# Kernel optimization log

Measured on AMD Instinct MI355X. Metric: run time of the kernel, lower is better.

Reference implementation:

```python
import jax, jax.numpy as jnp
import numpy as np

D_MODEL = 1024
N_HEADS = 16
N_KV_HEADS = 4
D_K = D_MODEL // N_HEADS  # 64
GROUPS = N_HEADS // N_KV_HEADS
GATE_IN = 12
Q_SIZE = D_MODEL
KV_SIZE = N_KV_HEADS * D_K
QKV_SIZE = Q_SIZE + 2 * KV_SIZE
ROPE_BASE = 10000.0


def rms_norm(x, w):
    # torch nn.RMSNorm with eps=None -> finfo(dtype).eps
    eps = jnp.finfo(x.dtype).eps
    var = jnp.mean(x * x, axis=-1, keepdims=True)
    return x * jax.lax.rsqrt(var + eps) * w


def rope(x):
    # torchtune RotaryPositionalEmbeddings: interleaved pairs. x: [B,S,H,D]
    B, S, H, D = x.shape
    half = D // 2
    theta = 1.0 / (ROPE_BASE ** (jnp.arange(0, half, dtype=jnp.float32) * 2.0 / D))
    ang = jnp.arange(S, dtype=jnp.float32)[:, None] * theta[None, :]  # [S, half]
    cos = jnp.cos(ang)[None, :, None, :]
    sin = jnp.sin(ang)[None, :, None, :]
    xp = x.reshape(B, S, H, half, 2)
    x0, x1 = xp[..., 0], xp[..., 1]
    out = jnp.stack([x0 * cos - x1 * sin, x1 * cos + x0 * sin], axis=-1)
    return out.reshape(B, S, H, D).astype(x.dtype)


def setup_inputs() -> dict:
    key = jax.random.key(0)
    k1, k2, k3, k4, k5 = jax.random.split(key, 5)
    B, S = 2, 2048
    x = jax.random.normal(k1, (B, S, D_MODEL), dtype=jnp.float32)
    qkvo_proj = 0.02 * jax.random.normal(k2, (QKV_SIZE + D_MODEL, D_MODEL), dtype=jnp.float32)
    q_norm_w = jnp.ones((D_K,), dtype=jnp.float32) + 0.01 * jax.random.normal(k3, (D_K,), dtype=jnp.float32)
    k_norm_w = jnp.ones((D_K,), dtype=jnp.float32) + 0.01 * jax.random.normal(k4, (D_K,), dtype=jnp.float32)
    gate_w = 0.02 * jax.random.normal(k5, (N_HEADS, GATE_IN), dtype=jnp.float32)
    return {"x": x, "qkvo_proj": qkvo_proj, "q_norm_w": q_norm_w,
            "k_norm_w": k_norm_w, "gate_w": gate_w}


def reference(x, qkvo_proj, q_norm_w, k_norm_w, gate_w):
    B, S, _ = x.shape
    qkv = jnp.einsum('bsd,ed->bse', x, qkvo_proj[:QKV_SIZE])
    Q = qkv[..., :Q_SIZE].reshape(B, S, N_HEADS, D_K)
    K = qkv[..., Q_SIZE:Q_SIZE + KV_SIZE].reshape(B, S, N_KV_HEADS, D_K)
    V = qkv[..., Q_SIZE + KV_SIZE:].reshape(B, S, N_KV_HEADS, D_K)
    Q = rope(rms_norm(Q, q_norm_w))
    K = rope(rms_norm(K, k_norm_w))
    # GQA: repeat kv heads (repeat_interleave along head dim)
    K = jnp.repeat(K, GROUPS, axis=2)
    V = jnp.repeat(V, GROUPS, axis=2)
    scale = 1.0 / jnp.sqrt(jnp.float32(D_K))
    scores = jnp.einsum('bqhd,bkhd->bhqk', Q, K) * scale
    causal = jnp.tril(jnp.ones((S, S), dtype=bool))
    scores = jnp.where(causal[None, None], scores, jnp.float32(-jnp.inf))
    probs = jax.nn.softmax(scores, axis=-1)
    attn = jnp.einsum('bhqk,bkhd->bqhd', probs, V)  # [B,S,H,D_K]
    gate = jax.nn.sigmoid(jnp.einsum('bsg,hg->bsh', x[..., :GATE_IN], gate_w))
    attn = attn * gate[..., None]
    attn = attn.reshape(B, S, D_MODEL)
    return jnp.einsum('bsd,ed->bse', attn, qkvo_proj[QKV_SIZE:])
```

## Files before the change

### kernel.cpp

```cpp
#include <hip/hip_runtime.h>
#include <math.h>

typedef unsigned short u16;
typedef unsigned int u32;
typedef __bf16 bf16x8 __attribute__((ext_vector_type(8)));
typedef float f32x4 __attribute__((ext_vector_type(4)));
typedef unsigned short u16x8 __attribute__((ext_vector_type(8)));
typedef unsigned int u32x2 __attribute__((ext_vector_type(2)));

static __device__ __forceinline__ u16 f2bf(float f) {
  unsigned int u = __builtin_bit_cast(unsigned int, f);
  u = (u + 0x7FFFu + ((u >> 16) & 1u)) >> 16;
  return (u16)u;
}
static __device__ __forceinline__ float bf2f(u16 u) {
  unsigned int x = ((unsigned int)u) << 16;
  return __builtin_bit_cast(float, x);
}
static __device__ __forceinline__ u16 f2bfh(float f) {
  __bf16 b = (__bf16)f;
  return __builtin_bit_cast(u16, b);
}
static __device__ __forceinline__ void gll16(const u16* g, u16* l) {
  __builtin_amdgcn_global_load_lds((const __attribute__((address_space(1))) u32*)g,
                                   (__attribute__((address_space(3))) u32*)l, 16, 0, 0);
}

#define QSCALE 0.18033688011112042f

__global__ __launch_bounds__(256) void prep_k(const float* __restrict__ a, u16* __restrict__ da, int n4a,
                                              const float* __restrict__ b, u16* __restrict__ db, int n4b,
                                              float2* __restrict__ tab) {
  int idx = blockIdx.x * 256 + threadIdx.x;
  if (idx < n4a + n4b) {
    const float* src; u16* dst; int i;
    if (idx < n4a) { src = a; dst = da; i = idx; }
    else { src = b; dst = db; i = idx - n4a; }
    float4 v = ((const float4*)src)[i];
    ushort4 r;
    r.x = f2bf(v.x); r.y = f2bf(v.y); r.z = f2bf(v.z); r.w = f2bf(v.w);
    ((ushort4*)dst)[i] = r;
  } else {
    int e = idx - n4a - n4b;
    if (e < 2048 * 32) {
      int s = e >> 5, j = e & 31;
      float sn, cs;
      sincosf((float)s * expf(-(float)j * (9.21034037198f / 32.0f)), &sn, &cs);
      tab[e] = make_float2(cs, sn);
    }
  }
}

__global__ __launch_bounds__(256) void gemm_nt(const u16* __restrict__ A, const u16* __restrict__ B,
                                               float* __restrict__ C, int M, int N, int K) {
  __shared__ __align__(16) u16 sA[64 * 32];
  __shared__ __align__(16) u16 sB[128 * 32];
  const int tid = threadIdx.x;
  const int w = tid >> 6, lane = tid & 63, l15 = lane & 15;
  const int m0 = blockIdx.x * 64, n0 = blockIdx.y * 128;
  const int wm = (w >> 1) * 32, wn = (w & 1) * 64;

  f32x4 acc[2][4] = {};

  int sArow, sAcol;
  {
    int p = tid * 16;
    int row = p >> 6, oo = p & 63;
    int ol = oo ^ (((row >> 1) & 3) << 4);
    sArow = row; sAcol = ol >> 1;
  }
  int sBrow[2], sBcol[2];
#pragma unroll
  for (int i = 0; i < 2; ++i) {
    int p = i * 4096 + tid * 16;
    int row = p >> 6, oo = p & 63;
    int ol = oo ^ (((row >> 1) & 3) << 4);
    sBrow[i] = row; sBcol[i] = ol >> 1;
  }
  int aoff[2], boff[4];
  const int kb = (lane >> 4) * 16;
#pragma unroll
  for (int m = 0; m < 2; ++m) {
    int r = wm + m * 16 + l15;
    aoff[m] = r * 64 + (kb ^ (((r >> 1) & 3) << 4));
  }
#pragma unroll
  for (int n = 0; n < 4; ++n) {
    int r = wn + n * 16 + l15;
    boff[n] = r * 64 + (kb ^ (((r >> 1) & 3) << 4));
  }

  for (int k0 = 0; k0 < K; k0 += 32) {
    gll16(A + (size_t)(m0 + sArow) * K + k0 + sAcol, (u16*)((char*)sA + tid * 16));
#pragma unroll
    for (int i = 0; i < 2; ++i)
      gll16(B + (size_t)(n0 + sBrow[i]) * K + k0 + sBcol[i], (u16*)((char*)sB + i * 4096 + tid * 16));
    __syncthreads();
    bf16x8 af[2], bfr[4];
#pragma unroll
    for (int m = 0; m < 2; ++m) af[m] = *(const bf16x8*)((const char*)sA + aoff[m]);
#pragma unroll
    for (int n = 0; n < 4; ++n) bfr[n] = *(const bf16x8*)((const char*)sB + boff[n]);
#pragma unroll
    for (int m = 0; m < 2; ++m)
#pragma unroll
      for (int n = 0; n < 4; ++n)
        acc[m][n] = __builtin_amdgcn_mfma_f32_16x16x32_bf16(af[m], bfr[n], acc[m][n], 0, 0, 0);
    __syncthreads();
  }

#pragma unroll
  for (int m = 0; m < 2; ++m)
#pragma unroll
    for (int i = 0; i < 4; ++i) {
      int gr = m0 + wm + m * 16 + (lane >> 4) * 4 + i;
      float* crow = C + (size_t)gr * N + n0 + wn + l15;
#pragma unroll
      for (int n = 0; n < 4; ++n) crow[n * 16] = acc[m][n][i];
    }
}

__global__ __launch_bounds__(256) void gemm_qkv(const u16* __restrict__ A, const u16* __restrict__ B,
                                                const float* __restrict__ qw, const float* __restrict__ kw,
                                                const float2* __restrict__ tab,
                                                u16* __restrict__ Qo, u16* __restrict__ Ko,
                                                u16* __restrict__ Vt, int K) {
  __shared__ __align__(16) u16 sA[64 * 32];
  __shared__ __align__(16) u16 sB[128 * 32];
  const int tid = threadIdx.x;
  const int w = tid >> 6, lane = tid & 63, l15 = lane & 15, lg = lane >> 4;
  const int m0 = blockIdx.x * 64, n0 = blockIdx.y * 128;
  const int wm = (w >> 1) * 32, wn = (w & 1) * 64;

  f32x4 acc[2][4] = {};

  int sArow, sAcol;
  {
    int p = tid * 16;
    int row = p >> 6, oo = p & 63;
    int ol = oo ^ (((row >> 1) & 3) << 4);
    sArow = row; sAcol = ol >> 1;
  }
  int sBrow[2], sBcol[2];
#pragma unroll
  for (int i = 0; i < 2; ++i) {
    int p = i * 4096 + tid * 16;
    int row = p >> 6, oo = p & 63;
    int ol = oo ^ (((row >> 1) & 3) << 4);
    sBrow[i] = row; sBcol[i] = ol >> 1;
  }
  int aoff[2], boff[4];
  const int kb = lg * 16;
#pragma unroll
  for (int m = 0; m < 2; ++m) {
    int r = wm + m * 16 + l15;
    aoff[m] = r * 64 + (kb ^ (((r >> 1) & 3) << 4));
  }
#pragma unroll
  for (int n = 0; n < 4; ++n) {
    int r = wn + n * 16 + l15;
    boff[n] = r * 64 + (kb ^ (((r >> 1) & 3) << 4));
  }

  for (int k0 = 0; k0 < K; k0 += 32) {
    gll16(A + (size_t)(m0 + sArow) * K + k0 + sAcol, (u16*)((char*)sA + tid * 16));
#pragma unroll
    for (int i = 0; i < 2; ++i)
      gll16(B + (size_t)(n0 + sBrow[i]) * K + k0 + sBcol[i], (u16*)((char*)sB + i * 4096 + tid * 16));
    __syncthreads();
    bf16x8 af[2], bfr[4];
#pragma unroll
    for (int m = 0; m < 2; ++m) af[m] = *(const bf16x8*)((const char*)sA + aoff[m]);
#pragma unroll
    for (int n = 0; n < 4; ++n) bfr[n] = *(const bf16x8*)((const char*)sB + boff[n]);
#pragma unroll
    for (int m = 0; m < 2; ++m)
#pragma unroll
      for (int n = 0; n < 4; ++n)
        acc[m][n] = __builtin_amdgcn_mfma_f32_16x16x32_bf16(af[m], bfr[n], acc[m][n], 0, 0, 0);
    __syncthreads();
  }

  const int he = (n0 + wn) >> 6;
  if (he < 20) {
    const float* wnorm = (he < 16) ? qw : kw;
    const float oscale = (he < 16) ? QSCALE : 1.0f;
    float wv[4];
#pragma unroll
    for (int n = 0; n < 4; ++n) wv[n] = wnorm[n * 16 + l15];
    float2 tj[4];
#pragma unroll
    for (int m = 0; m < 2; ++m)
#pragma unroll
      for (int i = 0; i < 4; ++i) {
        const int gr = m0 + wm + m * 16 + lg * 4 + i;
        const int s = gr & 2047, bb = gr >> 11;
        float ss = 0.f;
#pragma unroll
        for (int n = 0; n < 4; ++n) ss += acc[m][n][i] * acc[m][n][i];
        ss += __shfl_xor(ss, 8); ss += __shfl_xor(ss, 4);
        ss += __shfl_xor(ss, 2); ss += __shfl_xor(ss, 1);
        const float r = rsqrtf(ss * (1.0f / 64.0f) + 1.1920929e-7f);
#pragma unroll
        for (int n = 0; n < 4; ++n) tj[n] = tab[s * 32 + n * 8 + (l15 >> 1)];
        u16* orow = (he < 16)
          ? Qo + ((size_t)(bb * 16 + he) * 2048 + s) * 64 + l15
          : Ko + ((size_t)(bb * 4 + (he - 16)) * 2048 + s) * 64 + l15;
#pragma unroll
        for (int n = 0; n < 4; ++n) {
          float xn = acc[m][n][i] * r * wv[n];
          float p = __shfl_xor(xn, 1);
          float outv = ((l15 & 1) == 0) ? (xn * tj[n].x - p * tj[n].y)
                                        : (xn * tj[n].x + p * tj[n].y);
          orow[n * 16] = f2bf(outv * oscale);
        }
      }
  } else {
#pragma unroll
    for (int m = 0; m < 2; ++m)
#pragma unroll
      for (int i = 0; i < 4; ++i) {
        const int gr = m0 + wm + m * 16 + lg * 4 + i;
        const int s = gr & 2047, bb = gr >> 11;
        u16* vcol = Vt + ((size_t)(bb * 4 + (he - 20)) * 64 + l15) * 2048 + s;
#pragma unroll
        for (int n = 0; n < 4; ++n) vcol[(size_t)n * 16 * 2048] = f2bf(acc[m][n][i]);
      }
  }
}

__global__ __launch_bounds__(256) void attn_fwd_pair(const u16* __restrict__ Q, const u16* __restrict__ Kg,
                                                     const u16* __restrict__ Vt,
                                                     u16* __restrict__ accP, float* __restrict__ lP) {
  __shared__ __align__(16) u16 sK[64 * 64];
  __shared__ __align__(16) u16 sV[64 * 64];
  __shared__ __align__(16) u16 sP[4][16 * 64];

  const int tid = threadIdx.x;
  const int w = tid >> 6, lane = tid & 63;
  const int l15 = lane & 15, lg = lane >> 4;
  const int qiA = blockIdx.x;
  const int qiB = 31 - qiA;
  const int z = blockIdx.z;
  const int bh = blockIdx.y, b = bh >> 4, h = bh & 15, kvh = h >> 2;

  const u16* Qp = Q + (size_t)(b * 16 + h) * 2048 * 64;
  const u16* Kp = Kg + (size_t)(b * 4 + kvh) * 2048 * 64;
  const u16* Vp = Vt + (size_t)(b * 4 + kvh) * 64 * 2048;

  const int q0s[2] = {qiA * 64, qiB * 64};
  bf16x8 qa[2][2];
#pragma unroll
  for (int s = 0; s < 2; ++s) {
    const u16* qrow = Qp + (size_t)(q0s[s] + w * 16 + l15) * 64 + lg * 8;
    qa[s][0] = *(const bf16x8*)qrow;
    qa[s][1] = *(const bf16x8*)(qrow + 32);
  }

  f32x4 acc[2][4] = {};
  float l_s[2] = {0.f, 0.f};

  const int srw = tid >> 2;
  const int scb = (tid & 3) * 32;
  const int swzS = (srw & 7) << 4;
  const int st0 = srw * 128 + (scb ^ swzS);
  const int st1 = srw * 128 + ((scb + 16) ^ swzS);
  const u16* kgp = Kp + (size_t)srw * 64 + (tid & 3) * 16;
  const u16* vgp = Vp + (size_t)srw * 2048 + (tid & 3) * 16;

  const int swzF = (l15 & 7) << 4;
  const int fo0 = (lg * 16) ^ swzF;
  const int fo1 = (64 + lg * 16) ^ swzF;

  u16x8 kr0 = *(const u16x8*)(kgp + (size_t)z * 64 * 64), kr1 = *(const u16x8*)(kgp + (size_t)z * 64 * 64 + 8);
  u16x8 vr0 = *(const u16x8*)(vgp + z * 64),              vr1 = *(const u16x8*)(vgp + z * 64 + 8);

  for (int t = z; t <= qiB; t += 2) {
    __syncthreads();
    *(u16x8*)((char*)sK + st0) = kr0; *(u16x8*)((char*)sK + st1) = kr1;
    *(u16x8*)((char*)sV + st0) = vr0; *(u16x8*)((char*)sV + st1) = vr1;
    __syncthreads();

    if (t + 2 <= qiB) {
      const u16* kg = kgp + (size_t)(t + 2) * 64 * 64;
      const u16* vg = vgp + (t + 2) * 64;
      kr0 = *(const u16x8*)kg; kr1 = *(const u16x8*)(kg + 8);
      vr0 = *(const u16x8*)vg; vr1 = *(const u16x8*)(vg + 8);
    }

    bf16x8 kf[4][2], vf[4][2];
#pragma unroll
    for (int ct = 0; ct < 4; ++ct) {
      const char* krow = (const char*)sK + (ct * 16 + l15) * 128;
      const char* vrow = (const char*)sV + (ct * 16 + l15) * 128;
      kf[ct][0] = *(const bf16x8*)(krow + fo0);
      kf[ct][1] = *(const bf16x8*)(krow + fo1);
      vf[ct][0] = *(const bf16x8*)(vrow + fo0);
      vf[ct][1] = *(const bf16x8*)(vrow + fo1);
    }

#pragma unroll
    for (int s = 0; s < 2; ++s) {
      if (s == 0 && t > qiA) continue;
      const int diag = s ? qiB : qiA;

      f32x4 st[4];
#pragma unroll
      for (int ct = 0; ct < 4; ++ct) {
        f32x4 s4 = {};
        s4 = __builtin_amdgcn_mfma_f32_16x16x32_bf16(kf[ct][0], qa[s][0], s4, 0, 0, 0);
        s4 = __builtin_amdgcn_mfma_f32_16x16x32_bf16(kf[ct][1], qa[s][1], s4, 0, 0, 0);
        st[ct] = s4;
      }

      if (t == diag) {
        const int ql = w * 16 + l15;
#pragma unroll
        for (int ct = 0; ct < 4; ++ct)
#pragma unroll
          for (int i = 0; i < 4; ++i)
            st[ct][i] = (ct * 16 + lg * 4 + i <= ql) ? st[ct][i] : -1e30f;
      }

      float ls = 0.f;
      const int swzP = (l15 & 7) << 4;
      char* prow = (char*)sP[w] + l15 * 128;
#pragma unroll
      for (int ct = 0; ct < 4; ++ct) {
        float p0 = exp2f(st[ct][0]), p1 = exp2f(st[ct][1]);
        float p2 = exp2f(st[ct][2]), p3 = exp2f(st[ct][3]);
        ls += (p0 + p1) + (p2 + p3);
        u32 lo = (u32)f2bfh(p0) | ((u32)f2bfh(p1) << 16);
        u32 hi = (u32)f2bfh(p2) | ((u32)f2bfh(p3) << 16);
        *(u32x2*)(prow + ((ct * 32 + lg * 8) ^ swzP)) = (u32x2){lo, hi};
      }
      l_s[s] += ls;

      bf16x8 pa0 = *(const bf16x8*)(prow + ((lg * 16) ^ swzP));
      bf16x8 pa1 = *(const bf16x8*)(prow + ((64 + lg * 16) ^ swzP));

#pragma unroll
      for (int n = 0; n < 4; ++n) {
        acc[s][n] = __builtin_amdgcn_mfma_f32_16x16x32_bf16(pa0, vf[n][0], acc[s][n], 0, 0, 0);
        acc[s][n] = __builtin_amdgcn_mfma_f32_16x16x32_bf16(pa1, vf[n][1], acc[s][n], 0, 0, 0);
      }
    }
  }

#pragma unroll
  for (int s = 0; s < 2; ++s) {
    float lv = l_s[s];
    lv += __shfl_xor(lv, 16);
    lv += __shfl_xor(lv, 32);
    if (lg == 0) {
      int qrow = q0s[s] + w * 16 + l15;
      lP[((size_t)z * 4096 + b * 2048 + qrow) * 16 + h] = lv;
    }
#pragma unroll
    for (int i = 0; i < 4; ++i) {
      int srowg = q0s[s] + w * 16 + lg * 4 + i;
      size_t rowbase = (size_t)z * 4096 + b * 2048 + srowg;
      u16* orow = accP + rowbase * 1024 + h * 64 + l15;
#pragma unroll
      for (int n = 0; n < 4; ++n) orow[n * 16] = f2bfh(acc[s][n][i]);
    }
  }
}

__global__ __launch_bounds__(256) void attn_combine(const u16* __restrict__ accP, const float* __restrict__ lP,
                                                    const float* __restrict__ x, const float* __restrict__ gw,
                                                    u16* __restrict__ attnh) {
  const size_t e = ((size_t)blockIdx.x * 256 + threadIdx.x) * 8;
  const int token = (int)(e >> 10);
  const int h = (int)((e >> 6) & 15);
  u16x8 a0 = *(const u16x8*)(accP + e);
  u16x8 a1 = *(const u16x8*)(accP + ((size_t)4096 << 10) + e);
  const size_t li = (size_t)token * 16 + h;
  float l = lP[li] + lP[(size_t)4096 * 16 + li];
  float gd = 0.f;
#pragma unroll
  for (int j = 0; j < 12; ++j) gd += x[(size_t)token * 1024 + j] * gw[h * 12 + j];
  float g = (1.0f / (1.0f + __expf(-gd))) / l;
  u16x8 o;
#pragma unroll
  for (int j = 0; j < 8; ++j) o[j] = f2bfh((bf2f(a0[j]) + bf2f(a1[j])) * g);
  *(u16x8*)(attnh + e) = o;
}

extern "C" void kernel_launch(void* const* d_in, const int* in_sizes, int n_in,
                              void* d_out, int out_size, void* d_ws, size_t ws_size,
                              hipStream_t stream) {
  const float* x  = (const float*)d_in[0];
  const float* Wf = (const float*)d_in[1];
  const float* qw = (const float*)d_in[2];
  const float* kw = (const float*)d_in[3];
  const float* gw = (const float*)d_in[4];
  float* out = (float*)d_out;

  char* ws = (char*)d_ws;
  size_t off = 0;
  auto alloc = [&](size_t bytes) { void* p = ws + off; off += (bytes + 255) & ~(size_t)255; return p; };

  u16*    xb   = (u16*)alloc((size_t)4096 * 1024 * 2);
  u16*    wb   = (u16*)alloc((size_t)2560 * 1024 * 2);
  float2* tab  = (float2*)alloc((size_t)2048 * 32 * 8);
  u16*    Qb   = (u16*)alloc((size_t)2 * 16 * 2048 * 64 * 2);
  u16*    Kb   = (u16*)alloc((size_t)2 * 4 * 2048 * 64 * 2);
  u16*    Vtb  = (u16*)alloc((size_t)2 * 4 * 2048 * 64 * 2);
  float*  lP   = (float*)alloc((size_t)2 * 4096 * 16 * 4);
  u16*    accP = (u16*)alloc((size_t)2 * 4096 * 1024 * 2);
  u16* attnh = xb;

  const int n4a = 4096 * 1024 / 4, n4b = 2560 * 1024 / 4;
  const int prep_total = n4a + n4b + 2048 * 32;
  prep_k<<<dim3((prep_total + 255) / 256), dim3(256), 0, stream>>>(x, xb, n4a, Wf, wb, n4b, tab);
  gemm_qkv<<<dim3(64, 12), dim3(256), 0, stream>>>(xb, wb, qw, kw, tab, Qb, Kb, Vtb, 1024);
  attn_fwd_pair<<<dim3(16, 32, 2), dim3(256), 0, stream>>>(Qb, Kb, Vtb, accP, lP);
  attn_combine<<<dim3(2048), dim3(256), 0, stream>>>(accP, lP, x, gw, attnh);
  gemm_nt<<<dim3(64, 8), dim3(256), 0, stream>>>(attnh, wb + (size_t)1536 * 1024, out, 4096, 1024, 1024);
}
```

Before: 112.9 us.

## Double-buffer GEMM LDS tiles and fuse attention combine into output projection

The QKV GEMM now double-buffers its LDS tiles, prefetching the next K-slice while the current one feeds the MFMAs, so each iteration waits on one barrier instead of two. The separate combine kernel is removed: a small kernel computes the per-token, per-head gate divided by the softmax denominator, and the output GEMM sums the two partial attention buffers, scales them and converts to bf16 while loading its A tile. This avoids writing and re-reading the intermediate bf16 attention tensor. In exchange the output GEMM reads two A inputs through registers instead of async global-to-LDS loads, and uses twice the LDS.

```diff
diff --git a/kernel.cpp b/kernel.cpp
--- a/kernel.cpp
+++ b/kernel.cpp
@@ -51,12 +51,15 @@
   }
 }
 
-__global__ __launch_bounds__(256) void gemm_nt(const u16* __restrict__ A, const u16* __restrict__ B,
-                                               float* __restrict__ C, int M, int N, int K) {
-  __shared__ __align__(16) u16 sA[64 * 32];
-  __shared__ __align__(16) u16 sB[128 * 32];
+__global__ __launch_bounds__(256) void gemm_qkv(const u16* __restrict__ A, const u16* __restrict__ B,
+                                                const float* __restrict__ qw, const float* __restrict__ kw,
+                                                const float2* __restrict__ tab,
+                                                u16* __restrict__ Qo, u16* __restrict__ Ko,
+                                                u16* __restrict__ Vt, int K) {
+  __shared__ __align__(16) u16 sA[2][64 * 32];
+  __shared__ __align__(16) u16 sB[2][128 * 32];
   const int tid = threadIdx.x;
-  const int w = tid >> 6, lane = tid & 63, l15 = lane & 15;
+  const int w = tid >> 6, lane = tid & 63, l15 = lane & 15, lg = lane >> 4;
   const int m0 = blockIdx.x * 64, n0 = blockIdx.y * 128;
   const int wm = (w >> 1) * 32, wn = (w & 1) * 64;
 
@@ -78,7 +81,7 @@
     sBrow[i] = row; sBcol[i] = ol >> 1;
   }
   int aoff[2], boff[4];
-  const int kb = (lane >> 4) * 16;
+  const int kb = lg * 16;
 #pragma unroll
   for (int m = 0; m < 2; ++m) {
     int r = wm + m * 16 + l15;
@@ -90,95 +93,33 @@
     boff[n] = r * 64 + (kb ^ (((r >> 1) & 3) << 4));
   }
 
+  gll16(A + (size_t)(m0 + sArow) * K + sAcol, (u16*)((char*)sA[0] + tid * 16));
+#pragma unroll
+  for (int i = 0; i < 2; ++i)
+    gll16(B + (size_t)(n0 + sBrow[i]) * K + sBcol[i], (u16*)((char*)sB[0] + i * 4096 + tid * 16));
+  __syncthreads();
+
+  int cur = 0;
   for (int k0 = 0; k0 < K; k0 += 32) {
-    gll16(A + (size_t)(m0 + sArow) * K + k0 + sAcol, (u16*)((char*)sA + tid * 16));
-#pragma unroll
-    for (int i = 0; i < 2; ++i)
-      gll16(B + (size_t)(n0 + sBrow[i]) * K + k0 + sBcol[i], (u16*)((char*)sB + i * 4096 + tid * 16));
-    __syncthreads();
+    if (k0 + 32 < K) {
+      gll16(A + (size_t)(m0 + sArow) * K + (k0 + 32) + sAcol, (u16*)((char*)sA[cur ^ 1] + tid * 16));
+#pragma unroll
+      for (int i = 0; i < 2; ++i)
+        gll16(B + (size_t)(n0 + sBrow[i]) * K + (k0 + 32) + sBcol[i],
+              (u16*)((char*)sB[cur ^ 1] + i * 4096 + tid * 16));
+    }
     bf16x8 af[2], bfr[4];
 #pragma unroll
-    for (int m = 0; m < 2; ++m) af[m] = *(const bf16x8*)((const char*)sA + aoff[m]);
-#pragma unroll
-    for (int n = 0; n < 4; ++n) bfr[n] = *(const bf16x8*)((const char*)sB + boff[n]);
+    for (int m = 0; m < 2; ++m) af[m] = *(const bf16x8*)((const char*)sA[cur] + aoff[m]);
+#pragma unroll
+    for (int n = 0; n < 4; ++n) bfr[n] = *(const bf16x8*)((const char*)sB[cur] + boff[n]);
 #pragma unroll
     for (int m = 0; m < 2; ++m)
 #pragma unroll
       for (int n = 0; n < 4; ++n)
         acc[m][n] = __builtin_amdgcn_mfma_f32_16x16x32_bf16(af[m], bfr[n], acc[m][n], 0, 0, 0);
     __syncthreads();
-  }
-
-#pragma unroll
-  for (int m = 0; m < 2; ++m)
-#pragma unroll
-    for (int i = 0; i < 4; ++i) {
-      int gr = m0 + wm + m * 16 + (lane >> 4) * 4 + i;
-      float* crow = C + (size_t)gr * N + n0 + wn + l15;
-#pragma unroll
-      for (int n = 0; n < 4; ++n) crow[n * 16] = acc[m][n][i];
-    }
-}
-
-__global__ __launch_bounds__(256) void gemm_qkv(const u16* __restrict__ A, const u16* __restrict__ B,
-                                                const float* __restrict__ qw, const float* __restrict__ kw,
-                                                const float2* __restrict__ tab,
-                                                u16* __restrict__ Qo, u16* __restrict__ Ko,
-                                                u16* __restrict__ Vt, int K) {
-  __shared__ __align__(16) u16 sA[64 * 32];
-  __shared__ __align__(16) u16 sB[128 * 32];
-  const int tid = threadIdx.x;
-  const int w = tid >> 6, lane = tid & 63, l15 = lane & 15, lg = lane >> 4;
-  const int m0 = blockIdx.x * 64, n0 = blockIdx.y * 128;
-  const int wm = (w >> 1) * 32, wn = (w & 1) * 64;
-
-  f32x4 acc[2][4] = {};
-
-  int sArow, sAcol;
-  {
-    int p = tid * 16;
-    int row = p >> 6, oo = p & 63;
-    int ol = oo ^ (((row >> 1) & 3) << 4);
-    sArow = row; sAcol = ol >> 1;
-  }
-  int sBrow[2], sBcol[2];
-#pragma unroll
-  for (int i = 0; i < 2; ++i) {
-    int p = i * 4096 + tid * 16;
-    int row = p >> 6, oo = p & 63;
-    int ol = oo ^ (((row >> 1) & 3) << 4);
-    sBrow[i] = row; sBcol[i] = ol >> 1;
-  }
-  int aoff[2], boff[4];
-  const int kb = lg * 16;
-#pragma unroll
-  for (int m = 0; m < 2; ++m) {
-    int r = wm + m * 16 + l15;
-    aoff[m] = r * 64 + (kb ^ (((r >> 1) & 3) << 4));
-  }
-#pragma unroll
-  for (int n = 0; n < 4; ++n) {
-    int r = wn + n * 16 + l15;
-    boff[n] = r * 64 + (kb ^ (((r >> 1) & 3) << 4));
-  }
-
-  for (int k0 = 0; k0 < K; k0 += 32) {
-    gll16(A + (size_t)(m0 + sArow) * K + k0 + sAcol, (u16*)((char*)sA + tid * 16));
-#pragma unroll
-    for (int i = 0; i < 2; ++i)
-      gll16(B + (size_t)(n0 + sBrow[i]) * K + k0 + sBcol[i], (u16*)((char*)sB + i * 4096 + tid * 16));
-    __syncthreads();
-    bf16x8 af[2], bfr[4];
-#pragma unroll
-    for (int m = 0; m < 2; ++m) af[m] = *(const bf16x8*)((const char*)sA + aoff[m]);
-#pragma unroll
-    for (int n = 0; n < 4; ++n) bfr[n] = *(const bf16x8*)((const char*)sB + boff[n]);
-#pragma unroll
-    for (int m = 0; m < 2; ++m)
-#pragma unroll
-      for (int n = 0; n < 4; ++n)
-        acc[m][n] = __builtin_amdgcn_mfma_f32_16x16x32_bf16(af[m], bfr[n], acc[m][n], 0, 0, 0);
-    __syncthreads();
+    cur ^= 1;
   }
 
   const int he = (n0 + wn) >> 6;
@@ -367,24 +308,111 @@
   }
 }
 
-__global__ __launch_bounds__(256) void attn_combine(const u16* __restrict__ accP, const float* __restrict__ lP,
-                                                    const float* __restrict__ x, const float* __restrict__ gw,
-                                                    u16* __restrict__ attnh) {
-  const size_t e = ((size_t)blockIdx.x * 256 + threadIdx.x) * 8;
-  const int token = (int)(e >> 10);
-  const int h = (int)((e >> 6) & 15);
-  u16x8 a0 = *(const u16x8*)(accP + e);
-  u16x8 a1 = *(const u16x8*)(accP + ((size_t)4096 << 10) + e);
-  const size_t li = (size_t)token * 16 + h;
-  float l = lP[li] + lP[(size_t)4096 * 16 + li];
+__global__ __launch_bounds__(256) void invg_k(const float* __restrict__ lP, const float* __restrict__ x,
+                                              const float* __restrict__ gw, float* __restrict__ ivg) {
+  int i = blockIdx.x * 256 + threadIdx.x;
+  int token = i >> 4, h = i & 15;
+  float l = lP[i] + lP[4096 * 16 + i];
   float gd = 0.f;
 #pragma unroll
   for (int j = 0; j < 12; ++j) gd += x[(size_t)token * 1024 + j] * gw[h * 12 + j];
-  float g = (1.0f / (1.0f + __expf(-gd))) / l;
-  u16x8 o;
-#pragma unroll
-  for (int j = 0; j < 8; ++j) o[j] = f2bfh((bf2f(a0[j]) + bf2f(a1[j])) * g);
-  *(u16x8*)(attnh + e) = o;
+  ivg[i] = (1.0f / (1.0f + __expf(-gd))) / l;
+}
+
+__global__ __launch_bounds__(256) void gemm_out(const u16* __restrict__ accP, const float* __restrict__ ivg,
+                                                const u16* __restrict__ B, float* __restrict__ C,
+                                                int N, int K) {
+  __shared__ __align__(16) u16 sA[2][64 * 32];
+  __shared__ __align__(16) u16 sB[2][128 * 32];
+  const int tid = threadIdx.x;
+  const int w = tid >> 6, lane = tid & 63, l15 = lane & 15;
+  const int m0 = blockIdx.x * 64, n0 = blockIdx.y * 128;
+  const int wm = (w >> 1) * 32, wn = (w & 1) * 64;
+
+  f32x4 acc[2][4] = {};
+
+  const int sArow = tid >> 2;
+  const int scolA = ((((tid & 3) * 16) ^ (((sArow >> 1) & 3) << 4)) >> 1);
+  const int tokenA = m0 + sArow;
+  const u16* a0p = accP + (size_t)tokenA * 1024;
+  const u16* a1p = accP + (size_t)(4096 + tokenA) * 1024;
+
+  int sBrow[2], sBcol[2];
+#pragma unroll
+  for (int i = 0; i < 2; ++i) {
+    int p = i * 4096 + tid * 16;
+    int row = p >> 6, oo = p & 63;
+    int ol = oo ^ (((row >> 1) & 3) << 4);
+    sBrow[i] = row; sBcol[i] = ol >> 1;
+  }
+  int aoff[2], boff[4];
+  const int kb = (lane >> 4) * 16;
+#pragma unroll
+  for (int m = 0; m < 2; ++m) {
+    int r = wm + m * 16 + l15;
+    aoff[m] = r * 64 + (kb ^ (((r >> 1) & 3) << 4));
+  }
+#pragma unroll
+  for (int n = 0; n < 4; ++n) {
+    int r = wn + n * 16 + l15;
+    boff[n] = r * 64 + (kb ^ (((r >> 1) & 3) << 4));
+  }
+
+  auto loadA = [&](int k0) -> u16x8 {
+    const int e = k0 + scolA;
+    const float g = ivg[tokenA * 16 + (e >> 6)];
+    u16x8 a0 = *(const u16x8*)(a0p + e);
+    u16x8 a1 = *(const u16x8*)(a1p + e);
+    u16x8 r;
+#pragma unroll
+    for (int j = 0; j < 8; ++j) r[j] = f2bf((bf2f(a0[j]) + bf2f(a1[j])) * g);
+    return r;
+  };
+
+  {
+    u16x8 va = loadA(0);
+    *(u16x8*)((char*)sA[0] + tid * 16) = va;
+  }
+#pragma unroll
+  for (int i = 0; i < 2; ++i)
+    gll16(B + (size_t)(n0 + sBrow[i]) * K + sBcol[i], (u16*)((char*)sB[0] + i * 4096 + tid * 16));
+  __syncthreads();
+
+  int cur = 0;
+  for (int k0 = 0; k0 < K; k0 += 32) {
+    u16x8 va;
+    const bool more = (k0 + 32 < K);
+    if (more) {
+#pragma unroll
+      for (int i = 0; i < 2; ++i)
+        gll16(B + (size_t)(n0 + sBrow[i]) * K + (k0 + 32) + sBcol[i],
+              (u16*)((char*)sB[cur ^ 1] + i * 4096 + tid * 16));
+      va = loadA(k0 + 32);
+    }
+    bf16x8 af[2], bfr[4];
+#pragma unroll
+    for (int m = 0; m < 2; ++m) af[m] = *(const bf16x8*)((const char*)sA[cur] + aoff[m]);
+#pragma unroll
+    for (int n = 0; n < 4; ++n) bfr[n] = *(const bf16x8*)((const char*)sB[cur] + boff[n]);
+#pragma unroll
+    for (int m = 0; m < 2; ++m)
+#pragma unroll
+      for (int n = 0; n < 4; ++n)
+        acc[m][n] = __builtin_amdgcn_mfma_f32_16x16x32_bf16(af[m], bfr[n], acc[m][n], 0, 0, 0);
+    if (more) *(u16x8*)((char*)sA[cur ^ 1] + tid * 16) = va;
+    __syncthreads();
+    cur ^= 1;
+  }
+
+#pragma unroll
+  for (int m = 0; m < 2; ++m)
+#pragma unroll
+    for (int i = 0; i < 4; ++i) {
+      int gr = m0 + wm + m * 16 + (lane >> 4) * 4 + i;
+      float* crow = C + (size_t)gr * N + n0 + wn + l15;
+#pragma unroll
+      for (int n = 0; n < 4; ++n) crow[n * 16] = acc[m][n][i];
+    }
 }
 
 extern "C" void kernel_launch(void* const* d_in, const int* in_sizes, int n_in,
@@ -409,13 +437,13 @@
   u16*    Vtb  = (u16*)alloc((size_t)2 * 4 * 2048 * 64 * 2);
   float*  lP   = (float*)alloc((size_t)2 * 4096 * 16 * 4);
   u16*    accP = (u16*)alloc((size_t)2 * 4096 * 1024 * 2);
-  u16* attnh = xb;
+  float*  ivg  = (float*)alloc((size_t)4096 * 16 * 4);
 
   const int n4a = 4096 * 1024 / 4, n4b = 2560 * 1024 / 4;
   const int prep_total = n4a + n4b + 2048 * 32;
   prep_k<<<dim3((prep_total + 255) / 256), dim3(256), 0, stream>>>(x, xb, n4a, Wf, wb, n4b, tab);
   gemm_qkv<<<dim3(64, 12), dim3(256), 0, stream>>>(xb, wb, qw, kw, tab, Qb, Kb, Vtb, 1024);
   attn_fwd_pair<<<dim3(16, 32, 2), dim3(256), 0, stream>>>(Qb, Kb, Vtb, accP, lP);
-  attn_combine<<<dim3(2048), dim3(256), 0, stream>>>(accP, lP, x, gw, attnh);
-  gemm_nt<<<dim3(64, 8), dim3(256), 0, stream>>>(attnh, wb + (size_t)1536 * 1024, out, 4096, 1024, 1024);
-}
+  invg_k<<<dim3(256), dim3(256), 0, stream>>>(lP, x, gw, ivg);
+  gemm_out<<<dim3(64, 8), dim3(256), 0, stream>>>(accP, ivg, wb + (size_t)1536 * 1024, out, 1024, 1024);
+}
```

Measured after the change: 115.7 us. 2.5% more time.
